# Kernel optimization log

Hardware: AMD Instinct MI355X
Metric: run time of the kernel (lower is better)

The kernel has to match this reference:

```python
import jax, jax.numpy as jnp
import numpy as np

NX, NY = 128, 128
NT = 50
DECAY = 0.1
M1 = M2 = 12
WIDTH = 64


def _spectral(x, w1, w2):
    # x: [B, W, NX, NY]; w1/w2: complex [W, W, M1, M2]
    xf = jnp.fft.rfft2(x)                                   # [B, W, NX, NY//2+1]
    of = jnp.zeros(xf.shape[:2] + (NX, NY // 2 + 1), jnp.complex64)
    of = of.at[:, :, :M1, :M2].set(jnp.einsum('bixy,ioxy->boxy', xf[:, :, :M1, :M2], w1))
    of = of.at[:, :, NX - M1:, :M2].set(jnp.einsum('bixy,ioxy->boxy', xf[:, :, NX - M1:, :M2], w2))
    return jnp.fft.irfft2(of, s=(NX, NY))


def _forward(xyt_q, obs_coords, obs_vals, x_grid, y_grid,
             fc0_w, fc0_b, spec_w1r, spec_w1i, spec_w2r, spec_w2i,
             pw_w, pw_b, fc1_w, fc1_b, fc2_w, fc2_b,
             nb_idx, sensor_iy, sensor_ix, Lx, Ly):
    B, K = nb_idx.shape
    # ---- gather obs, temporal-decay weight, scatter-add into sparse grid ----
    sensor_ids = nb_idx // NT                               # [B, K]
    t_nb = obs_coords[nb_idx, 2]                            # [B, K]
    w = jnp.exp(-DECAY * jnp.abs(t_nb - xyt_q[:, None, 2])) # [B, K]
    vals = obs_vals[nb_idx] * w                             # [B, K]
    lin = sensor_iy[sensor_ids] * NY + sensor_ix[sensor_ids]
    flat = (lin + jnp.arange(B)[:, None] * (NX * NY)).ravel()
    sparse = jnp.zeros(B * NX * NY, obs_vals.dtype).at[flat].add(vals.ravel())
    counts = jnp.zeros(B * NX * NY, obs_vals.dtype).at[flat].add(w.ravel())
    grid = jnp.where(counts > 0, sparse / jnp.maximum(counts, 1e-6), 0.0).reshape(B, NX, NY)
    # ---- FNO core ----
    inp = jnp.stack([grid,
                     jnp.broadcast_to(x_grid, (B, NX, NY)),
                     jnp.broadcast_to(y_grid, (B, NX, NY))], axis=1)  # [B, 3, NX, NY]
    x = jnp.einsum('bcxy,cw->bwxy', inp, fc0_w) + fc0_b[None, :, None, None]
    for i in range(4):
        y = (_spectral(x, spec_w1r[i] + 1j * spec_w1i[i], spec_w2r[i] + 1j * spec_w2i[i])
             + jnp.einsum('bcxy,oc->boxy', x, pw_w[i]) + pw_b[i][None, :, None, None])
        x = jax.nn.gelu(y, approximate=False) if i < 3 else y
    h = jax.nn.gelu(jnp.einsum('bwxy,wf->bxyf', x, fc1_w) + fc1_b, approximate=False)
    field = (jnp.einsum('bxyf,fo->bxyo', h, fc2_w) + fc2_b).transpose(0, 3, 1, 2)  # [B, 3, NX, NY]
    # ---- bilinear sample at query points ----
    x01 = jnp.clip(xyt_q[:, 0] / max(Lx, 1e-6), 0.0, 1.0)
    y01 = jnp.clip(xyt_q[:, 1] / max(Ly, 1e-6), 0.0, 1.0)
    gx = x01 * (NX - 1)
    gy = y01 * (NY - 1)
    x0 = jnp.floor(gx).astype(jnp.int32)
    y0 = jnp.floor(gy).astype(jnp.int32)
    x1 = jnp.minimum(x0 + 1, NX - 1)
    y1 = jnp.minimum(y0 + 1, NY - 1)
    wx = (gx - x0)[:, None]
    wy = (gy - y0)[:, None]
    b = jnp.arange(B)
    f00 = field[b, :, x0, y0]
    f10 = field[b, :, x1, y0]
    f01 = field[b, :, x0, y1]
    f11 = field[b, :, x1, y1]
    top = f00 * (1.0 - wx) + f10 * wx
    bot = f01 * (1.0 - wx) + f11 * wx
    return top * (1.0 - wy) + bot * wy                       # [B, 3]


def setup_inputs() -> dict:
    key = jax.random.key(0)
    ks = jax.random.split(key, 20)
    B, K, NOBS, NS = 64, 64, 50000, 1000
    scale = 1.0 / (WIDTH * WIDTH)
    inp = {
        'xyt_q': jax.random.uniform(ks[0], (B, 3), jnp.float32),
        'obs_coords': jax.random.uniform(ks[1], (NOBS, 3), jnp.float32),
        'obs_vals': jax.random.normal(ks[2], (NOBS,), jnp.float32),
        'x_grid': jax.random.uniform(ks[3], (NX, NY), jnp.float32),
        'y_grid': jax.random.uniform(ks[4], (NX, NY), jnp.float32),
        'fc0_w': jax.random.normal(ks[5], (3, WIDTH), jnp.float32) * 0.3,
        'fc0_b': jnp.zeros((WIDTH,), jnp.float32),
        'spec_w1r': scale * jax.random.uniform(ks[6], (4, WIDTH, WIDTH, M1, M2), jnp.float32),
        'spec_w1i': scale * jax.random.uniform(ks[7], (4, WIDTH, WIDTH, M1, M2), jnp.float32),
        'spec_w2r': scale * jax.random.uniform(ks[8], (4, WIDTH, WIDTH, M1, M2), jnp.float32),
        'spec_w2i': scale * jax.random.uniform(ks[9], (4, WIDTH, WIDTH, M1, M2), jnp.float32),
        'pw_w': jax.random.normal(ks[10], (4, WIDTH, WIDTH), jnp.float32) * (1.0 / np.sqrt(WIDTH)),
        'pw_b': jnp.zeros((4, WIDTH), jnp.float32),
        'fc1_w': jax.random.normal(ks[11], (WIDTH, 128), jnp.float32) * (1.0 / np.sqrt(WIDTH)),
        'fc1_b': jnp.zeros((128,), jnp.float32),
        'fc2_w': jax.random.normal(ks[12], (128, 3), jnp.float32) * (1.0 / np.sqrt(128.0)),
        'fc2_b': jnp.zeros((3,), jnp.float32),
        'nb_idx': jax.random.randint(ks[13], (B, K), 0, NOBS, jnp.int32),
        'sensor_iy': jax.random.randint(ks[14], (NS,), 0, NX, jnp.int32),
        'sensor_ix': jax.random.randint(ks[15], (NS,), 0, NY, jnp.int32),
        'Lx': 1,
        'Ly': 1,
    }
    return inp


def reference(xyt_q, obs_coords, obs_vals, x_grid, y_grid,
              fc0_w, fc0_b, spec_w1r, spec_w1i, spec_w2r, spec_w2i,
              pw_w, pw_b, fc1_w, fc1_b, fc2_w, fc2_b,
              nb_idx, sensor_iy, sensor_ix, Lx, Ly):
    return _forward(xyt_q, obs_coords, obs_vals, x_grid, y_grid,
                    fc0_w, fc0_b, spec_w1r, spec_w1i, spec_w2r, spec_w2i,
                    pw_w, pw_b, fc1_w, fc1_b, fc2_w, fc2_b,
                    nb_idx, sensor_iy, sensor_ix, Lx, Ly)
```

## Files before the change

### kernel.cpp

```cpp
#include <hip/hip_runtime.h>
#include <math.h>

#define NXg 128
#define NYg 128
#define Pg  (NXg*NYg)
#define Bq  64
#define Wd  64
#define NKX 24
#define NMODE (NKX*12)
#define PI2_128 0.04908738521234052f

typedef _Float16 f16x8 __attribute__((ext_vector_type(8)));
typedef _Float16 f16x4 __attribute__((ext_vector_type(4)));
typedef float    f32x4 __attribute__((ext_vector_type(4)));

#define OFF_TC  0
#define OFF_TS  (OFF_TC + 128)
#define F32_END (OFF_TS + 128)
#define H_T1E  0
#define H_T1ET (H_T1E + 32*128)
#define H_A2   (H_T1ET + 128*32)
#define H_PWH  (H_A2 + 48*256)
#define H_T2ET (H_PWH + 4*64*64)
#define H_XFHR (H_T2ET + 128*64)
#define H_XFHI (H_XFHR + 288*4096)
#define H_OFHR (H_XFHI + 288*4096)
#define H_OFHI (H_OFHR + 288*4096)
#define H_WHR  (H_OFHI + 288*4096)
#define H_WHI  (H_WHR + (size_t)4*288*4096)
#define H_YG   (H_WHI + (size_t)4*288*4096)
#define H_X    (H_YG + (size_t)Bq*Wd*128*24)
#define H_U    (H_X + (size_t)Bq*128*128*64)

__device__ __forceinline__ float fast_gelu(float v) {
    float a = fabsf(v) * 0.70710678118654752f;
    float t = 1.f / (1.f + 0.3275911f * a);
    float p = t * (0.254829592f + t * (-0.284496736f + t * (1.421413741f +
              t * (-1.453152027f + t * 1.061405429f))));
    float er = 1.f - p * __expf(-a * a);
    er = copysignf(er, v);
    return 0.5f * v * (1.f + er);
}

__global__ void k_prep(_Float16* T1e_g, _Float16* T1eT_g, _Float16* A2_g,
                       const float* pww, _Float16* PWh, _Float16* T2eT_g,
                       float* Tc, float* Ts,
                       const float* xyt, const float* obs_c, const float* obs_v,
                       const int* nb, const int* siy, const int* six,
                       float* val, float* cnt,
                       const float* w1r, const float* w1i,
                       const float* w2r, const float* w2i,
                       _Float16* Whr, _Float16* Whi) {
    int blk = blockIdx.x;
    if (blk < 64) {
        int t = blk * 256 + threadIdx.x;
        if (t < 32*128) {
            int r = t >> 7, y = t & 127;
            float v = 0.f;
            if (r < 12)      v =  cosf((float)((r * y) & 127) * PI2_128);
            else if (r < 24) v = -sinf((float)(((r-12) * y) & 127) * PI2_128);
            T1e_g[t] = (_Float16)v;
            int y2 = t >> 5, r2 = t & 31;
            float v2 = 0.f;
            if (r2 < 12)      v2 =  cosf((float)((r2 * y2) & 127) * PI2_128);
            else if (r2 < 24) v2 = -sinf((float)(((r2-12) * y2) & 127) * PI2_128);
            T1eT_g[t] = (_Float16)v2;
        }
        if (t < 48*256) {
            int m = t >> 8, k = t & 255;
            int x = k & 127;
            int hi = (k >= 128);
            float v;
            if (m < 24) {
                int kx = (m < 12) ? m : (104 + m);
                float th = (float)((kx * x) & 127) * PI2_128;
                v = hi ? sinf(th) : cosf(th);
            } else {
                int mm = m - 24;
                int kx = (mm < 12) ? mm : (104 + mm);
                float th = (float)((kx * x) & 127) * PI2_128;
                v = hi ? cosf(th) : -sinf(th);
            }
            A2_g[t] = (_Float16)v;
        }
        if (t < 4*64*64) PWh[t] = (_Float16)pww[t];
        if (t < 128*64) {
            int x = t >> 6, k = t & 63;
            float v = 0.f;
            if (k < 24) {
                int kx = (k < 12) ? k : (104 + k);
                v = cosf((float)((kx * x) & 127) * PI2_128);
            } else if (k < 48) {
                int kk = k - 24;
                int kx = (kk < 12) ? kk : (104 + kk);
                v = sinf((float)((kx * x) & 127) * PI2_128);
            }
            T2eT_g[t] = (_Float16)v;
        }
        if (t < 128) {
            float th = (float)t * PI2_128;
            Tc[t] = cosf(th);
            Ts[t] = sinf(th);
        }
    } else if (blk < 80) {
        int t = (blk - 64) * 256 + threadIdx.x;
        int b = t >> 6;
        int id = nb[t];
        int sid = id / 50;
        float tq = xyt[b*3 + 2];
        float w = expf(-0.1f * fabsf(obs_c[id*3 + 2] - tq));
        int lin = siy[sid] * NYg + six[sid];
        atomicAdd(&val[b*Pg + lin], obs_v[id] * w);
        atomicAdd(&cnt[b*Pg + lin], w);
    } else {
        int u = blk - 80;
        int layer = u / 288, mode = u - layer*288;
        int kxi = mode / 12, ky = mode - kxi*12;
        const float *wr, *wi; int kxw;
        if (kxi < 12) { wr = w1r; wi = w1i; kxw = kxi; }
        else          { wr = w2r; wi = w2i; kxw = kxi - 12; }
        size_t obase = (size_t)(layer*288 + mode) * 4096;
        size_t lbase = (size_t)layer * 64*64*144 + (size_t)kxw*12 + ky;
        for (int k = 0; k < 16; k++) {
            int p = k*256 + threadIdx.x;
            int o = p >> 6, i = p & 63;
            size_t widx = lbase + (size_t)(i*64 + o)*144;
            Whr[obase + p] = (_Float16)wr[widx];
            Whi[obase + p] = (_Float16)wi[widx];
        }
    }
}

__device__ __forceinline__ void stageA(const _Float16 (*Xn)[76], const _Float16* __restrict__ T1e_g,
                                       _Float16* __restrict__ Yg, int b, int row, int tid) {
    int wave = tid >> 6, lane = tid & 63;
    int l15 = lane & 15, quad = lane >> 4;
    f16x8 bf[8];
    #pragma unroll
    for (int u = 0; u < 8; u++) {
        int nt2 = u >> 2, q = u & 3;
        bf[u] = *(const f16x8*)&T1e_g[(nt2*16 + l15)*128 + q*32 + quad*8];
    }
    f16x8 af[4];
    #pragma unroll
    for (int q = 0; q < 4; q++)
        #pragma unroll
        for (int j = 0; j < 8; j++)
            af[q][j] = Xn[q*32 + quad*8 + j][wave*16 + l15];
    #pragma unroll
    for (int nt2 = 0; nt2 < 2; nt2++) {
        f32x4 acc = {0.f,0.f,0.f,0.f};
        #pragma unroll
        for (int q = 0; q < 4; q++)
            acc = __builtin_amdgcn_mfma_f32_16x16x32_f16(af[q], bf[nt2*4 + q], acc, 0, 0, 0);
        int t = nt2*16 + l15;
        if (t < 24) {
            #pragma unroll
            for (int r = 0; r < 4; r++) {
                int o = wave*16 + quad*4 + r;
                Yg[((size_t)(b*64 + o)*128 + row)*24 + t] = (_Float16)acc[r];
            }
        }
    }
}

__global__ __launch_bounds__(256) void k_fc0y(const float* __restrict__ val, const float* __restrict__ cnt,
                      const float* __restrict__ xg, const float* __restrict__ yg,
                      const float* __restrict__ w, const float* __restrict__ bb,
                      const _Float16* __restrict__ T1e_g,
                      _Float16* __restrict__ Yg) {
    __shared__ _Float16 Xn[128][76];
    __shared__ float wl[4][64];
    int row = blockIdx.x, b = blockIdx.y;
    int tid = threadIdx.x;
    if (tid < 64) {
        wl[0][tid] = w[tid]; wl[1][tid] = w[64+tid]; wl[2][tid] = w[128+tid]; wl[3][tid] = bb[tid];
    }
    __syncthreads();
    {
        int y = tid & 127, half = tid >> 7;
        int p = row*128 + y;
        float c = cnt[(size_t)b*Pg + p];
        float g = (c > 0.f) ? val[(size_t)b*Pg + p] / fmaxf(c, 1e-6f) : 0.f;
        float a1 = xg[p], a2 = yg[p];
        #pragma unroll
        for (int blk = 0; blk < 4; blk++) {
            f16x8 pk;
            #pragma unroll
            for (int j = 0; j < 8; j++) {
                int o = half*32 + blk*8 + j;
                pk[j] = (_Float16)(g*wl[0][o] + a1*wl[1][o] + a2*wl[2][o] + wl[3][o]);
            }
            *(f16x8*)&Xn[y][half*32 + blk*8] = pk;
        }
    }
    __syncthreads();
    stageA(Xn, T1e_g, Yg, b, row, tid);
}

__global__ __launch_bounds__(256) void k_sB(const _Float16* __restrict__ Yg,
                    const _Float16* __restrict__ A2_g,
                    _Float16* __restrict__ xfhr, _Float16* __restrict__ xfhi) {
    __shared__ _Float16 Ys[28][136];
    int bc = blockIdx.x;
    int tid = threadIdx.x;
    int wave = tid >> 6, lane = tid & 63;
    int l15 = lane & 15, quad = lane >> 4;
    const _Float16* base = Yg + (size_t)bc * 3072;
    for (int i = tid; i < 3072; i += 256) {
        int x = i / 24, t = i - x*24;
        Ys[t][x] = base[i];
    }
    __syncthreads();
    if (wave < 3) {
        f32x4 acc = {0.f,0.f,0.f,0.f};
        #pragma unroll
        for (int q = 0; q < 8; q++) {
            f16x8 a = *(const f16x8*)&A2_g[(size_t)(wave*16 + l15)*256 + q*32 + quad*8];
            const _Float16* brow = (q < 4) ? &Ys[l15][q*32 + quad*8]
                                           : &Ys[12 + l15][(q-4)*32 + quad*8];
            f16x8 bfr = *(const f16x8*)brow;
            acc = __builtin_amdgcn_mfma_f32_16x16x32_f16(a, bfr, acc, 0, 0, 0);
        }
        if (l15 < 12) {
            #pragma unroll
            for (int r = 0; r < 4; r++) {
                int m = wave*16 + quad*4 + r;
                if (m < 24) xfhr[(size_t)(m*12 + l15)*4096 + bc] = (_Float16)acc[r];
                else        xfhi[(size_t)((m-24)*12 + l15)*4096 + bc] = (_Float16)acc[r];
            }
        }
    }
}

__global__ __launch_bounds__(256) void k_s3m(const _Float16* __restrict__ xfhr, const _Float16* __restrict__ xfhi,
                    const _Float16* __restrict__ Whr, const _Float16* __restrict__ Whi,
                    _Float16* __restrict__ ofhr, _Float16* __restrict__ ofhi, int layer) {
    __shared__ _Float16 Xr[64][72], Xi[64][72];
    int mode = blockIdx.x;
    int tid = threadIdx.x;
    int wave = tid >> 6, lane = tid & 63;
    int l15 = lane & 15, quad = lane >> 4;
    const _Float16* pr = xfhr + (size_t)mode * 4096;
    const _Float16* pi = xfhi + (size_t)mode * 4096;
    for (int c8 = tid; c8 < 512; c8 += 256) {
        int b = c8 >> 3, seg = c8 & 7;
        *(f16x8*)&Xr[b][seg*8] = *(const f16x8*)&pr[c8*8];
        *(f16x8*)&Xi[b][seg*8] = *(const f16x8*)&pi[c8*8];
    }
    __syncthreads();
    size_t wb = ((size_t)(layer*288 + mode)*64 + wave*16 + l15) * 64 + quad*8;
    f16x8 wr0 = *(const f16x8*)&Whr[wb];
    f16x8 wr1 = *(const f16x8*)&Whr[wb + 32];
    f16x8 wi0 = *(const f16x8*)&Whi[wb];
    f16x8 wi1 = *(const f16x8*)&Whi[wb + 32];
    #pragma unroll
    for (int mt = 0; mt < 4; mt++) {
        f16x8 xr0 = *(const f16x8*)&Xr[mt*16 + l15][quad*8];
        f16x8 xr1 = *(const f16x8*)&Xr[mt*16 + l15][32 + quad*8];
        f16x8 xi0 = *(const f16x8*)&Xi[mt*16 + l15][quad*8];
        f16x8 xi1 = *(const f16x8*)&Xi[mt*16 + l15][32 + quad*8];
        f16x8 xn0, xn1;
        #pragma unroll
        for (int j = 0; j < 8; j++) { xn0[j] = -xi0[j]; xn1[j] = -xi1[j]; }
        f32x4 cr = {0.f,0.f,0.f,0.f}, ci = {0.f,0.f,0.f,0.f};
        cr = __builtin_amdgcn_mfma_f32_16x16x32_f16(xr0, wr0, cr, 0, 0, 0);
        cr = __builtin_amdgcn_mfma_f32_16x16x32_f16(xr1, wr1, cr, 0, 0, 0);
        cr = __builtin_amdgcn_mfma_f32_16x16x32_f16(xn0, wi0, cr, 0, 0, 0);
        cr = __builtin_amdgcn_mfma_f32_16x16x32_f16(xn1, wi1, cr, 0, 0, 0);
        ci = __builtin_amdgcn_mfma_f32_16x16x32_f16(xr0, wi0, ci, 0, 0, 0);
        ci = __builtin_amdgcn_mfma_f32_16x16x32_f16(xr1, wi1, ci, 0, 0, 0);
        ci = __builtin_amdgcn_mfma_f32_16x16x32_f16(xi0, wr0, ci, 0, 0, 0);
        ci = __builtin_amdgcn_mfma_f32_16x16x32_f16(xi1, wr1, ci, 0, 0, 0);
        #pragma unroll
        for (int r = 0; r < 4; r++) {
            int b = mt*16 + quad*4 + r;
            int o = wave*16 + l15;
            ofhr[(size_t)mode*4096 + b*64 + o] = (_Float16)cr[r];
            ofhi[(size_t)mode*4096 + b*64 + o] = (_Float16)ci[r];
        }
    }
}

__global__ __launch_bounds__(256) void k_sG(const _Float16* __restrict__ ofhr, const _Float16* __restrict__ ofhi,
                    const _Float16* __restrict__ T2eT_g, _Float16* __restrict__ Gh) {
    __shared__ _Float16 As[64][72];
    __shared__ _Float16 Cs[128][72];
    int b = blockIdx.x, t = blockIdx.y;
    int tid = threadIdx.x;
    int wave = tid >> 6, lane = tid & 63;
    int l15 = lane & 15, quad = lane >> 4;
    int ky = (t < 12) ? t : (t - 12);
    float sc = ((ky == 0) ? 1.f : 2.f) * (1.f/16384.f);
    bool isReal = (t < 12);
    for (int i = tid; i < 1536; i += 256) {
        int kxi = i >> 6, o = i & 63;
        size_t idx = (size_t)(kxi*12 + ky)*4096 + b*64 + o;
        float vr = (float)ofhr[idx] * sc, vi = (float)ofhi[idx] * sc;
        As[o][kxi]      = (_Float16)(isReal ? vr : vi);
        As[o][24 + kxi] = (_Float16)(isReal ? -vi : vr);
    }
    for (int i = tid; i < 1024; i += 256)
        As[i >> 4][48 + (i & 15)] = (_Float16)0.f;
    __syncthreads();
    f16x8 a0 = *(const f16x8*)&As[wave*16 + l15][quad*8];
    f16x8 a1 = *(const f16x8*)&As[wave*16 + l15][32 + quad*8];
    #pragma unroll
    for (int nt = 0; nt < 8; nt++) {
        f16x8 b0 = *(const f16x8*)&T2eT_g[(nt*16 + l15)*64 + quad*8];
        f16x8 b1 = *(const f16x8*)&T2eT_g[(nt*16 + l15)*64 + 32 + quad*8];
        f32x4 acc = {0.f,0.f,0.f,0.f};
        acc = __builtin_amdgcn_mfma_f32_16x16x32_f16(a0, b0, acc, 0, 0, 0);
        acc = __builtin_amdgcn_mfma_f32_16x16x32_f16(a1, b1, acc, 0, 0, 0);
        f16x4 pk;
        #pragma unroll
        for (int r = 0; r < 4; r++) pk[r] = (_Float16)acc[r];
        *(f16x4*)&Cs[nt*16 + l15][wave*16 + quad*4] = pk;
    }
    __syncthreads();
    _Float16* outp = Gh + ((size_t)(b*24 + t) << 13);
    float4* o4 = (float4*)outp;
    for (int i = tid; i < 1024; i += 256) {
        int x = i >> 3, seg = i & 7;
        o4[i] = *(const float4*)&Cs[x][seg*8];
    }
}

__global__ __launch_bounds__(256) void k_s45(_Float16* __restrict__ xh,
                    const _Float16* __restrict__ Gh,
                    const _Float16* __restrict__ T1e_g, const _Float16* __restrict__ T1eT_g,
                    const _Float16* __restrict__ PWh,
                    const float* __restrict__ pwb,
                    _Float16* __restrict__ Yg, int layer,
                    const float* __restrict__ xyt, const int* __restrict__ Lx,
                    const float* __restrict__ val, const float* __restrict__ cnt,
                    const float* __restrict__ xg, const float* __restrict__ yg,
                    const float* __restrict__ fc0w, const float* __restrict__ fc0b) {
    __shared__ _Float16 BsT[128][76];
    __shared__ float wl[4][64];
    int row = blockIdx.x, b = blockIdx.y;
    int tid = threadIdx.x;
    int wave = tid >> 6, lane = tid & 63;
    int l15 = lane & 15, quad = lane >> 4;

    _Float16* xrow = xh + (size_t)(b*128 + row) * 8192;

    f16x8 af0 = *(const f16x8*)&PWh[(size_t)(layer*64 + wave*16 + l15)*64 + quad*8];
    f16x8 af1 = *(const f16x8*)&PWh[(size_t)(layer*64 + wave*16 + l15)*64 + 32 + quad*8];
    f16x8 af2;
    #pragma unroll
    for (int j = 0; j < 8; j++) af2[j] = (_Float16)0.f;
    if (quad < 3) {
        const _Float16* gbase = Gh + ((size_t)(b*24 + quad*8)*128 + row)*64 + wave*16 + l15;
        #pragma unroll
        for (int j = 0; j < 8; j++) af2[j] = gbase[(size_t)j * 8192];
    }
    f16x8 b2a[8];
    #pragma unroll
    for (int nt = 0; nt < 8; nt++)
        b2a[nt] = *(const f16x8*)&T1eT_g[(nt*16 + l15)*32 + quad*8];
    float pb[4];
    #pragma unroll
    for (int r = 0; r < 4; r++)
        pb[r] = pwb[layer*64 + wave*16 + quad*4 + r];

    if (layer == 0) {
        if (tid < 64) {
            wl[0][tid] = fc0w[tid]; wl[1][tid] = fc0w[64+tid];
            wl[2][tid] = fc0w[128+tid]; wl[3][tid] = fc0b[tid];
        }
        __syncthreads();
        int y = tid & 127, half = tid >> 7;
        int p = row*128 + y;
        float c = cnt[(size_t)b*Pg + p];
        float g = (c > 0.f) ? val[(size_t)b*Pg + p] / fmaxf(c, 1e-6f) : 0.f;
        float a1 = xg[p], a2 = yg[p];
        #pragma unroll
        for (int blk = 0; blk < 4; blk++) {
            f16x8 pk;
            #pragma unroll
            for (int j = 0; j < 8; j++) {
                int o = half*32 + blk*8 + j;
                pk[j] = (_Float16)(g*wl[0][o] + a1*wl[1][o] + a2*wl[2][o] + wl[3][o]);
            }
            *(f16x8*)&BsT[y][half*32 + blk*8] = pk;
        }
    } else {
        const float4* xr4 = (const float4*)xrow;
        for (int i = tid; i < 1024; i += 256) {
            int y = i >> 3, seg = i & 7;
            *(float4*)&BsT[y][seg*8] = xr4[i];
        }
    }
    __syncthreads();

    f32x4 acc[8];
    #pragma unroll
    for (int nt = 0; nt < 8; nt++) {
        f32x4 a = {0.f,0.f,0.f,0.f};
        f16x8 b0 = *(const f16x8*)&BsT[nt*16 + l15][quad*8];
        f16x8 b1 = *(const f16x8*)&BsT[nt*16 + l15][32 + quad*8];
        a = __builtin_amdgcn_mfma_f32_16x16x32_f16(af0, b0, a, 0, 0, 0);
        a = __builtin_amdgcn_mfma_f32_16x16x32_f16(af1, b1, a, 0, 0, 0);
        a = __builtin_amdgcn_mfma_f32_16x16x32_f16(af2, b2a[nt], a, 0, 0, 0);
        acc[nt] = a;
    }
    __syncthreads();

    #pragma unroll
    for (int nt = 0; nt < 8; nt++) {
        int y = nt*16 + l15;
        f16x4 pk;
        #pragma unroll
        for (int r = 0; r < 4; r++) {
            float v = acc[nt][r] + pb[r];
            pk[r] = (_Float16)fast_gelu(v);
        }
        *(f16x4*)&BsT[y][wave*16 + quad*4] = pk;
    }
    __syncthreads();

    bool store_x = true;
    if (layer == 2) {
        float Lxf = fmaxf((float)Lx[0], 1e-6f);
        float x01 = fminf(fmaxf(xyt[b*3 + 0] / Lxf, 0.f), 1.f);
        float gxp = x01 * (NXg - 1);
        int x0 = (int)floorf(gxp);
        int x1 = min(x0 + 1, NXg - 1);
        store_x = (row == x0) || (row == x1);
    }
    if (store_x) {
        float4* xw4 = (float4*)xrow;
        for (int i = tid; i < 1024; i += 256) {
            int y = i >> 3, seg = i & 7;
            xw4[i] = *(const float4*)&BsT[y][seg*8];
        }
    }
    stageA(BsT, T1e_g, Yg, b, row, tid);
}

__global__ __launch_bounds__(256) void k_final(const _Float16* __restrict__ x,
                    const _Float16* __restrict__ ofhr, const _Float16* __restrict__ ofhi,
                    const float* __restrict__ pw, const float* __restrict__ pwb,
                    const float* __restrict__ fc1w, const float* __restrict__ fc1b,
                    const float* __restrict__ fc2w, const float* __restrict__ fc2b,
                    const float* __restrict__ xyt, const int* __restrict__ Lx, const int* __restrict__ Ly,
                    const float* __restrict__ Tc, const float* __restrict__ Ts,
                    float* __restrict__ out) {
    __shared__ float y4[4][64];
    __shared__ float hh[4][129];
    __shared__ int   pxy[4][2];
    __shared__ float wxy[2];
    __shared__ float tc[128], ts[128];
    int b = blockIdx.x;
    if (threadIdx.x < 128) {
        tc[threadIdx.x] = Tc[threadIdx.x];
        ts[threadIdx.x] = Ts[threadIdx.x];
    }
    if (threadIdx.x == 0) {
        float Lxf = fmaxf((float)Lx[0], 1e-6f);
        float Lyf = fmaxf((float)Ly[0], 1e-6f);
        float x01 = fminf(fmaxf(xyt[b*3 + 0] / Lxf, 0.f), 1.f);
        float y01 = fminf(fmaxf(xyt[b*3 + 1] / Lyf, 0.f), 1.f);
        float gx = x01 * (NXg - 1), gy = y01 * (NYg - 1);
        int x0 = (int)floorf(gx), y0 = (int)floorf(gy);
        int x1 = min(x0 + 1, NXg - 1), y1 = min(y0 + 1, NYg - 1);
        wxy[0] = gx - (float)x0;
        wxy[1] = gy - (float)y0;
        pxy[0][0] = x0; pxy[0][1] = y0;
        pxy[1][0] = x1; pxy[1][1] = y0;
        pxy[2][0] = x0; pxy[2][1] = y1;
        pxy[3][0] = x1; pxy[3][1] = y1;
    }
    __syncthreads();
    {
        int p = threadIdx.x >> 6, o = threadIdx.x & 63;
        int px = pxy[p][0], py = pxy[p][1];
        float gkr[12], gki[12];
        #pragma unroll
        for (int ky = 0; ky < 12; ky++) { gkr[ky] = 0.f; gki[ky] = 0.f; }
        for (int kxi = 0; kxi < 24; kxi++) {
            int kx = (kxi < 12) ? kxi : (104 + kxi);
            int m = (kx * px) & 127;
            float cc = tc[m], ss = ts[m];
            #pragma unroll
            for (int ky = 0; ky < 12; ky++) {
                size_t idx = (size_t)(kxi*12 + ky)*4096 + b*64 + o;
                float a = (float)ofhr[idx], bb = (float)ofhi[idx];
                gkr[ky] += a*cc - bb*ss;
                gki[ky] += a*ss + bb*cc;
            }
        }
        float sp = gkr[0];
        #pragma unroll
        for (int ky = 1; ky < 12; ky++) {
            int m = (ky * py) & 127;
            sp += 2.f * (gkr[ky]*tc[m] - gki[ky]*ts[m]);
        }
        float s = 0.f;
        const _Float16* xb = x + ((size_t)(b*128 + px)*128 + py)*64;
        #pragma unroll 4
        for (int c = 0; c < 64; c++)
            s += pw[3*4096 + o*64 + c] * (float)xb[c];
        y4[p][o] = sp * (1.f/16384.f) + s + pwb[3*64 + o];
    }
    __syncthreads();
    for (int i = threadIdx.x; i < 512; i += 256) {
        int p = i >> 7, f = i & 127;
        float s = fc1b[f];
        #pragma unroll 4
        for (int w = 0; w < 64; w++) s += y4[p][w] * fc1w[w*128 + f];
        hh[p][f] = 0.5f * s * (1.f + erff(s * 0.70710678118654752f));
    }
    __syncthreads();
    if (threadIdx.x < 3) {
        int o3 = threadIdx.x;
        float f4[4];
        #pragma unroll
        for (int p = 0; p < 4; p++) {
            float s = fc2b[o3];
            #pragma unroll 4
            for (int f = 0; f < 128; f++) s += hh[p][f] * fc2w[f*3 + o3];
            f4[p] = s;
        }
        float wx = wxy[0], wy = wxy[1];
        float top = f4[0]*(1.f - wx) + f4[1]*wx;
        float bot = f4[2]*(1.f - wx) + f4[3]*wx;
        out[b*3 + o3] = top*(1.f - wy) + bot*wy;
    }
}

extern "C" void kernel_launch(void* const* d_in, const int* in_sizes, int n_in,
                              void* d_out, int out_size, void* d_ws, size_t ws_size,
                              hipStream_t stream) {
    const float* xyt    = (const float*)d_in[0];
    const float* obs_c  = (const float*)d_in[1];
    const float* obs_v  = (const float*)d_in[2];
    const float* xg     = (const float*)d_in[3];
    const float* yg     = (const float*)d_in[4];
    const float* fc0w   = (const float*)d_in[5];
    const float* fc0b   = (const float*)d_in[6];
    const float* w1r    = (const float*)d_in[7];
    const float* w1i    = (const float*)d_in[8];
    const float* w2r    = (const float*)d_in[9];
    const float* w2i    = (const float*)d_in[10];
    const float* pww    = (const float*)d_in[11];
    const float* pwb    = (const float*)d_in[12];
    const float* fc1w   = (const float*)d_in[13];
    const float* fc1b   = (const float*)d_in[14];
    const float* fc2w   = (const float*)d_in[15];
    const float* fc2b   = (const float*)d_in[16];
    const int*   nb     = (const int*)d_in[17];
    const int*   siy    = (const int*)d_in[18];
    const int*   six    = (const int*)d_in[19];
    const int*   Lx     = (const int*)d_in[20];
    const int*   Ly     = (const int*)d_in[21];
    float* out = (float*)d_out;

    float* W = (float*)d_ws;
    float* Tc  = W + OFF_TC;
    float* Ts  = W + OFF_TS;
    _Float16* Hbase = (_Float16*)(W + F32_END);
    _Float16* T1e_g  = Hbase + H_T1E;
    _Float16* T1eT_g = Hbase + H_T1ET;
    _Float16* A2_g   = Hbase + H_A2;
    _Float16* PWh    = Hbase + H_PWH;
    _Float16* T2eT_g = Hbase + H_T2ET;
    _Float16* xfhr   = Hbase + H_XFHR;
    _Float16* xfhi   = Hbase + H_XFHI;
    _Float16* ofhr   = Hbase + H_OFHR;
    _Float16* ofhi   = Hbase + H_OFHI;
    _Float16* Whr    = Hbase + H_WHR;
    _Float16* Whi    = Hbase + H_WHI;
    _Float16* Yg     = Hbase + H_YG;
    _Float16* xh     = Hbase + H_X;
    float*    val    = (float*)(Hbase + H_U);
    float*    cnt    = val + Bq*Pg;
    _Float16* Gh     = Hbase + H_U;
    _Float16* Gh2    = Hbase + H_U + (size_t)4*Bq*Pg;

    hipMemsetAsync(val, 0, (size_t)2 * Bq * Pg * sizeof(float), stream);

    k_prep<<<1232, 256, 0, stream>>>(T1e_g, T1eT_g, A2_g, pww, PWh, T2eT_g, Tc, Ts,
                                     xyt, obs_c, obs_v, nb, siy, six, val, cnt,
                                     w1r, w1i, w2r, w2i, Whr, Whi);
    k_fc0y<<<dim3(128, Bq), 256, 0, stream>>>(val, cnt, xg, yg, fc0w, fc0b, T1e_g, Yg);

    for (int l = 0; l < 3; l++) {
        k_sB<<<Bq*Wd, 256, 0, stream>>>(Yg, A2_g, xfhr, xfhi);
        k_s3m<<<288, 256, 0, stream>>>(xfhr, xfhi, Whr, Whi, ofhr, ofhi, l);
        k_sG<<<dim3(Bq, 24), 256, 0, stream>>>(ofhr, ofhi, T2eT_g, Gh2);
        k_s45<<<dim3(128, Bq), 256, 0, stream>>>(xh, Gh2, T1e_g, T1eT_g, PWh, pwb, Yg, l,
                                                 xyt, Lx, val, cnt, xg, yg, fc0w, fc0b);
    }
    k_sB<<<Bq*Wd, 256, 0, stream>>>(Yg, A2_g, xfhr, xfhi);
    k_s3m<<<288, 256, 0, stream>>>(xfhr, xfhi, Whr, Whi, ofhr, ofhi, 3);
    k_final<<<Bq, 256, 0, stream>>>(xh, ofhr, ofhi, pww, pwb, fc1w, fc1b, fc2w, fc2b,
                                    xyt, Lx, Ly, Tc, Ts, out);
}
```

Before: 748.0 us.

## Coalesce weight conversion, vectorize Y transpose load, cut register pressure in s45

The spectral weight conversion in k_prep now reads the source weights contiguously as float4 and scatters fp16 values into the mode-major layout, using far fewer blocks than the previous strided-gather version. k_sB loads Yg as 8-wide vectors before transposing into shared memory. stageA and k_s45 load B fragments inside the MFMA loop instead of preloading them all, and k_s45 applies GELU immediately to hold packed fp16 results rather than fp32 accumulators. k_s45 also gets a launch-bounds occupancy hint of 7. The aim is lower register use, higher occupancy and coalesced memory access, at the cost of scattered 2-byte stores in prep and possibly less latency hiding for the B loads.

```diff
diff --git a/kernel.cpp b/kernel.cpp
--- a/kernel.cpp
+++ b/kernel.cpp
@@ -114,19 +114,27 @@
         atomicAdd(&cnt[b*Pg + lin], w);
     } else {
         int u = blk - 80;
-        int layer = u / 288, mode = u - layer*288;
-        int kxi = mode / 12, ky = mode - kxi*12;
-        const float *wr, *wi; int kxw;
-        if (kxi < 12) { wr = w1r; wi = w1i; kxw = kxi; }
-        else          { wr = w2r; wi = w2i; kxw = kxi - 12; }
-        size_t obase = (size_t)(layer*288 + mode) * 4096;
-        size_t lbase = (size_t)layer * 64*64*144 + (size_t)kxw*12 + ky;
+        int lt = u / 36;
+        int layer = lt >> 1, tens = lt & 1;
+        int cb = u - lt*36;
+        const float* srcr = (tens ? w2r : w1r) + (size_t)layer*589824 + cb*16384;
+        const float* srci = (tens ? w2i : w1i) + (size_t)layer*589824 + cb*16384;
+        int mbase = tens ? 144 : 0;
         for (int k = 0; k < 16; k++) {
-            int p = k*256 + threadIdx.x;
-            int o = p >> 6, i = p & 63;
-            size_t widx = lbase + (size_t)(i*64 + o)*144;
-            Whr[obase + p] = (_Float16)wr[widx];
-            Whi[obase + p] = (_Float16)wi[widx];
+            int p = k*1024 + threadIdx.x*4;
+            float4 vr = *(const float4*)&srcr[p];
+            float4 vi = *(const float4*)&srci[p];
+            int idx = cb*16384 + p;
+            #pragma unroll
+            for (int j = 0; j < 4; j++) {
+                int id = idx + j;
+                int ky = id % 12; int t2 = id / 12;
+                int kx = t2 % 12; int t3 = t2 / 12;
+                int o = t3 & 63;  int i = t3 >> 6;
+                size_t d = ((size_t)(layer*288 + mbase + kx*12 + ky))*4096 + o*64 + i;
+                Whr[d] = (_Float16)(&vr.x)[j];
+                Whi[d] = (_Float16)(&vi.x)[j];
+            }
         }
     }
 }
@@ -135,12 +143,6 @@
                                        _Float16* __restrict__ Yg, int b, int row, int tid) {
     int wave = tid >> 6, lane = tid & 63;
     int l15 = lane & 15, quad = lane >> 4;
-    f16x8 bf[8];
-    #pragma unroll
-    for (int u = 0; u < 8; u++) {
-        int nt2 = u >> 2, q = u & 3;
-        bf[u] = *(const f16x8*)&T1e_g[(nt2*16 + l15)*128 + q*32 + quad*8];
-    }
     f16x8 af[4];
     #pragma unroll
     for (int q = 0; q < 4; q++)
@@ -151,8 +153,10 @@
     for (int nt2 = 0; nt2 < 2; nt2++) {
         f32x4 acc = {0.f,0.f,0.f,0.f};
         #pragma unroll
-        for (int q = 0; q < 4; q++)
-            acc = __builtin_amdgcn_mfma_f32_16x16x32_f16(af[q], bf[nt2*4 + q], acc, 0, 0, 0);
+        for (int q = 0; q < 4; q++) {
+            f16x8 bf = *(const f16x8*)&T1e_g[(nt2*16 + l15)*128 + q*32 + quad*8];
+            acc = __builtin_amdgcn_mfma_f32_16x16x32_f16(af[q], bf, acc, 0, 0, 0);
+        }
         int t = nt2*16 + l15;
         if (t < 24) {
             #pragma unroll
@@ -207,9 +211,11 @@
     int wave = tid >> 6, lane = tid & 63;
     int l15 = lane & 15, quad = lane >> 4;
     const _Float16* base = Yg + (size_t)bc * 3072;
-    for (int i = tid; i < 3072; i += 256) {
-        int x = i / 24, t = i - x*24;
-        Ys[t][x] = base[i];
+    for (int i = tid; i < 384; i += 256) {
+        int x = i / 3, seg = i - x*3;
+        f16x8 v = *(const f16x8*)&base[x*24 + seg*8];
+        #pragma unroll
+        for (int j = 0; j < 8; j++) Ys[seg*8 + j][x] = v[j];
     }
     __syncthreads();
     if (wave < 3) {
@@ -326,7 +332,7 @@
     }
 }
 
-__global__ __launch_bounds__(256) void k_s45(_Float16* __restrict__ xh,
+__global__ __launch_bounds__(256, 7) void k_s45(_Float16* __restrict__ xh,
                     const _Float16* __restrict__ Gh,
                     const _Float16* __restrict__ T1e_g, const _Float16* __restrict__ T1eT_g,
                     const _Float16* __restrict__ PWh,
@@ -355,10 +361,6 @@
         #pragma unroll
         for (int j = 0; j < 8; j++) af2[j] = gbase[(size_t)j * 8192];
     }
-    f16x8 b2a[8];
-    #pragma unroll
-    for (int nt = 0; nt < 8; nt++)
-        b2a[nt] = *(const f16x8*)&T1eT_g[(nt*16 + l15)*32 + quad*8];
     float pb[4];
     #pragma unroll
     for (int r = 0; r < 4; r++)
@@ -394,30 +396,25 @@
     }
     __syncthreads();
 
-    f32x4 acc[8];
+    f16x4 pk[8];
     #pragma unroll
     for (int nt = 0; nt < 8; nt++) {
-        f32x4 a = {0.f,0.f,0.f,0.f};
         f16x8 b0 = *(const f16x8*)&BsT[nt*16 + l15][quad*8];
         f16x8 b1 = *(const f16x8*)&BsT[nt*16 + l15][32 + quad*8];
+        f16x8 b2 = *(const f16x8*)&T1eT_g[(nt*16 + l15)*32 + quad*8];
+        f32x4 a = {0.f,0.f,0.f,0.f};
         a = __builtin_amdgcn_mfma_f32_16x16x32_f16(af0, b0, a, 0, 0, 0);
         a = __builtin_amdgcn_mfma_f32_16x16x32_f16(af1, b1, a, 0, 0, 0);
-        a = __builtin_amdgcn_mfma_f32_16x16x32_f16(af2, b2a[nt], a, 0, 0, 0);
-        acc[nt] = a;
-    }
-    __syncthreads();
-
-    #pragma unroll
-    for (int nt = 0; nt < 8; nt++) {
-        int y = nt*16 + l15;
-        f16x4 pk;
-        #pragma unroll
-        for (int r = 0; r < 4; r++) {
-            float v = acc[nt][r] + pb[r];
-            pk[r] = (_Float16)fast_gelu(v);
-        }
-        *(f16x4*)&BsT[y][wave*16 + quad*4] = pk;
-    }
+        a = __builtin_amdgcn_mfma_f32_16x16x32_f16(af2, b2, a, 0, 0, 0);
+        #pragma unroll
+        for (int r = 0; r < 4; r++)
+            pk[nt][r] = (_Float16)fast_gelu(a[r] + pb[r]);
+    }
+    __syncthreads();
+
+    #pragma unroll
+    for (int nt = 0; nt < 8; nt++)
+        *(f16x4*)&BsT[nt*16 + l15][wave*16 + quad*4] = pk[nt];
     __syncthreads();
 
     bool store_x = true;
@@ -576,14 +573,13 @@
     _Float16* xh     = Hbase + H_X;
     float*    val    = (float*)(Hbase + H_U);
     float*    cnt    = val + Bq*Pg;
-    _Float16* Gh     = Hbase + H_U;
     _Float16* Gh2    = Hbase + H_U + (size_t)4*Bq*Pg;
 
     hipMemsetAsync(val, 0, (size_t)2 * Bq * Pg * sizeof(float), stream);
 
-    k_prep<<<1232, 256, 0, stream>>>(T1e_g, T1eT_g, A2_g, pww, PWh, T2eT_g, Tc, Ts,
-                                     xyt, obs_c, obs_v, nb, siy, six, val, cnt,
-                                     w1r, w1i, w2r, w2i, Whr, Whi);
+    k_prep<<<368, 256, 0, stream>>>(T1e_g, T1eT_g, A2_g, pww, PWh, T2eT_g, Tc, Ts,
+                                    xyt, obs_c, obs_v, nb, siy, six, val, cnt,
+                                    w1r, w1i, w2r, w2i, Whr, Whi);
     k_fc0y<<<dim3(128, Bq), 256, 0, stream>>>(val, cnt, xg, yg, fc0w, fc0b, T1e_g, Yg);
 
     for (int l = 0; l < 3; l++) {
```

Result: no change. 751.1 us (+0.4%).
